# Kernel optimization log

Hardware: AMD Instinct MI355X
Metric: run time of the kernel (lower is better)

Reference implementation:

```python
import jax, jax.numpy as jnp
import numpy as np

N, C, F, T, H = 8, 64, 256, 256, 64


def _ln(x, g, b, eps=1e-5):
    m = x.mean(-1, keepdims=True)
    v = x.var(-1, keepdims=True)  # biased var, matches torch LayerNorm
    return (x - m) * jax.lax.rsqrt(v + eps) * g + b


def setup_inputs() -> dict:
    key = jax.random.key(0)
    ks = jax.random.split(key, 8)
    s = 1.0 / np.sqrt(C)
    return {
        "inputs": jax.random.normal(ks[0], (N, C, F, T), jnp.float32),
        "Wq": jax.random.normal(ks[1], (H, C), jnp.float32) * s,
        "bq": jnp.zeros((H,), jnp.float32),
        "Wk": jax.random.normal(ks[2], (H, C), jnp.float32) * s,
        "bk": jnp.zeros((H,), jnp.float32),
        "Wv": jax.random.normal(ks[3], (H, C), jnp.float32) * s,
        "bv": jnp.zeros((H,), jnp.float32),
        "g1": jnp.ones((C,), jnp.float32),
        "b1": jnp.zeros((C,), jnp.float32),
        "g2": jnp.ones((H,), jnp.float32),
        "b2": jnp.zeros((H,), jnp.float32),
        "Wt": jax.random.normal(ks[4], (C, H), jnp.float32) * s,
        "bt": jnp.zeros((C,), jnp.float32),
        "g3": jnp.ones((C,), jnp.float32),
        "b3": jnp.zeros((C,), jnp.float32),
        "alpha": jnp.full((1,), 0.25, jnp.float32),
    }


def reference(inputs, Wq, bq, Wk, bk, Wv, bv, g1, b1, g2, b2, Wt, bt, g3, b3, alpha):
    n, c, f, t = inputs.shape
    # [N,C,F,T] -> [N*T, F, C]: attention over freq bins, channels as features
    x = inputs.transpose(0, 3, 2, 1).reshape(n * t, f, c)
    h = _ln(x, g1, b1)
    q = h @ Wq.T + bq  # [B, F, H]
    k = h @ Wk.T + bk
    v = h @ Wv.T + bv
    scale = 1.0 / jnp.sqrt(jnp.asarray(q.shape[-1], q.dtype))
    e = jnp.einsum('bth,bsh->bts', q, k) * scale  # [B, F, F]
    a = jax.nn.softmax(e, axis=-1)
    wv = jnp.einsum('bts,bsh->bth', a, v)
    wv = _ln(wv, g2, b2)
    out = wv @ Wt.T + bt  # [B, F, C]
    out = out.reshape(n, t, f, c)
    out = _ln(out, g3, b3)  # LayerNorm over channel dim
    out = jnp.where(out >= 0, out, alpha * out)  # PReLU (single param)
    out = out.transpose(0, 3, 2, 1)  # back to [N, C, F, T]
    return out + inputs  # dropout is identity in eval mode
```

## Files before the change

### kernel.cpp

```cpp
#include <hip/hip_runtime.h>

typedef _Float16 f16;
typedef _Float16 f16x2 __attribute__((ext_vector_type(2)));
typedef _Float16 f16x8 __attribute__((ext_vector_type(8)));
typedef float f32x16 __attribute__((ext_vector_type(16)));
typedef unsigned int u32;
typedef unsigned short u16;

#define MFMA(a, b, c) __builtin_amdgcn_mfma_f32_32x32x16_f16((a), (b), (c), 0, 0, 0)

__device__ __forceinline__ u32 pk2(float a, float b) {
  union { f16x2 h; u32 u; } x;
  x.h[0] = (f16)a; x.h[1] = (f16)b;
  return x.u;
}
__device__ __forceinline__ float2 up2(u32 u) {
  union { u32 u_; f16x2 h; } x; x.u_ = u;
  return make_float2((float)x.h[0], (float)x.h[1]);
}
__device__ __forceinline__ f16x8 mk8(u32 a, u32 b, u32 c, u32 d) {
  union { u32 u[4]; f16x8 v; } x;
  x.u[0] = a; x.u[1] = b; x.u[2] = c; x.u[3] = d;
  return x.v;
}
__device__ __forceinline__ u16 f16b(float v) {
  union { f16 h; u16 u; } x; x.h = (f16)v; return x.u;
}
__device__ __forceinline__ float ex2(float x) {
#if __has_builtin(__builtin_amdgcn_exp2f)
  return __builtin_amdgcn_exp2f(x);
#else
  return exp2f(x);
#endif
}

__device__ __forceinline__ void sp2(float a, float b, float S, u32* hi, u32* lo) {
  union { f16x2 h; u32 u; } xh, xl;
  xh.h[0] = (f16)a; xh.h[1] = (f16)b;
  float ra = (a - (float)xh.h[0]) * S;
  float rb = (b - (float)xh.h[1]) * S;
  xl.h[0] = (f16)ra; xl.h[1] = (f16)rb;
  *hi = xh.u; *lo = xl.u;
}

template<int CTRL>
__device__ __forceinline__ float dpp_add(float v) {
  int t = __builtin_amdgcn_update_dpp(0, __builtin_bit_cast(int, v), CTRL, 0xF, 0xF, true);
  return v + __builtin_bit_cast(float, t);
}
__device__ __forceinline__ float red32(float v) {
  v = dpp_add<0xB1>(v);
  v = dpp_add<0x4E>(v);
  v = dpp_add<0x141>(v);
  v = dpp_add<0x140>(v);
  int sw = __builtin_amdgcn_ds_swizzle(__builtin_bit_cast(int, v), 0x401F);
  return v + __builtin_bit_cast(float, sw);
}

__device__ __forceinline__ f16x8 xfrag(const f32x16 a, int kt1, int g5) {
  u32 u0, u1, u2, u3;
  if (kt1 == 0) {
    u0 = pk2(a[0], a[1]);   u1 = pk2(a[2], a[3]);
    u2 = pk2(a[4], a[5]);   u3 = pk2(a[6], a[7]);
  } else {
    u0 = pk2(a[8], a[9]);   u1 = pk2(a[10], a[11]);
    u2 = pk2(a[12], a[13]); u3 = pk2(a[14], a[15]);
  }
  u32 s0 = (u32)__shfl_xor((int)u0, 32);
  u32 s1 = (u32)__shfl_xor((int)u1, 32);
  u32 s2 = (u32)__shfl_xor((int)u2, 32);
  u32 s3 = (u32)__shfl_xor((int)u3, 32);
  u32 r0 = g5 ? s2 : u0;
  u32 r1 = g5 ? s3 : u1;
  u32 r2 = g5 ? u2 : s0;
  u32 r3 = g5 ? u3 : s1;
  return mk8(r0, r1, r2, r3);
}

__device__ __forceinline__ void xfrag2(const f32x16 a, int kt1, int g5,
                                       f16x8* hi, f16x8* lo, float S) {
  u32 uh[4], ul[4];
#pragma unroll
  for (int j = 0; j < 4; ++j) {
    float v0 = kt1 ? a[8 + 2 * j] : a[2 * j];
    float v1 = kt1 ? a[9 + 2 * j] : a[2 * j + 1];
    sp2(v0, v1, S, &uh[j], &ul[j]);
  }
  u32 sh[4], sl[4];
#pragma unroll
  for (int j = 0; j < 4; ++j) {
    sh[j] = (u32)__shfl_xor((int)uh[j], 32);
    sl[j] = (u32)__shfl_xor((int)ul[j], 32);
  }
  *hi = mk8(g5 ? sh[2] : uh[0], g5 ? sh[3] : uh[1],
            g5 ? uh[2] : sh[0], g5 ? uh[3] : sh[1]);
  *lo = mk8(g5 ? sl[2] : ul[0], g5 ? sl[3] : ul[1],
            g5 ? ul[2] : sl[0], g5 ? ul[3] : sl[1]);
}

__device__ __forceinline__ f16x8 ldfrag(const char* plane, int row, int kt, int g5) {
  int s = row & 15;
  int c8 = 4 * kt + 2 * g5;
  uint2 a = *(const uint2*)(plane + row * 128 + ((c8) ^ s) * 8);
  uint2 b = *(const uint2*)(plane + row * 128 + ((c8 + 1) ^ s) * 8);
  return mk8(a.x, a.y, b.x, b.y);
}

__global__ __launch_bounds__(256) void k_pre32(const float* __restrict__ inp,
                                               float* __restrict__ xws) {
  __shared__ float tile[64 * 65];
  const int bid = blockIdx.x;
  const int n = bid >> 10;
  const int rem = bid & 1023;
  const int f = rem >> 2;
  const int t0 = (rem & 3) << 6;
  const int tid = threadIdx.x;

  const int tt = tid & 63, cb = tid >> 6;
  const float* src = inp + ((size_t)n * 64 * 256 + f) * 256 + t0;
#pragma unroll
  for (int k = 0; k < 16; ++k) {
    int c = cb * 16 + k;
    tile[c * 65 + tt] = src[(size_t)c * 65536 + tt];
  }
  __syncthreads();
  const int c2 = (tid & 31) * 2, tb = tid >> 5;
#pragma unroll
  for (int k = 0; k < 8; ++k) {
    int t = tb + 8 * k;
    float2 v = make_float2(tile[c2 * 65 + t], tile[(c2 + 1) * 65 + t]);
    *(float2*)(xws + ((size_t)(n * 256 + t0 + t) * 256 + f) * 64 + c2) = v;
  }
}

__global__ __launch_bounds__(512, 2) void k_attn(
    const float* __restrict__ xg,
    u16* __restrict__ yws,
    const float* __restrict__ Wq, const float* __restrict__ bq,
    const float* __restrict__ Wk, const float* __restrict__ bk,
    const float* __restrict__ Wv, const float* __restrict__ bv,
    const float* __restrict__ g1, const float* __restrict__ b1,
    const float* __restrict__ g2, const float* __restrict__ b2,
    const float* __restrict__ Wt, const float* __restrict__ bt,
    const float* __restrict__ g3, const float* __restrict__ b3,
    const float* __restrict__ alp) {
  extern __shared__ char smem[];
  char* Khi = smem;
  char* Klo = smem + 32768;
  char* Vlds = smem + 65536;
  char* WkH = smem + 98304;
  char* WkL = smem + 106496;
  char* WvH = smem + 114688;
  char* WvL = smem + 122880;
  char* WqH = smem + 131072;
  char* WqL = smem + 139264;
  char* WtH = smem + 147456;

  const int tid = threadIdx.x;
  const int w = tid >> 6;
  const int lane = tid & 63;
  const int l31 = lane & 31;
  const int g5 = lane >> 5;
  const int l7 = l31 & 7;
  const int b = blockIdx.x;
  const float* xb = xg + (size_t)b * 16384;
  const float RLO = 1.f / 512.f;

  float xv[32];
  {
    int f = 32 * w + l31;
#pragma unroll
    for (int kt = 0; kt < 4; ++kt) {
      float4 a = *(const float4*)(xb + f * 64 + 16 * kt + 8 * g5);
      float4 c = *(const float4*)(xb + f * 64 + 16 * kt + 8 * g5 + 4);
      xv[kt * 8 + 0] = a.x; xv[kt * 8 + 1] = a.y;
      xv[kt * 8 + 2] = a.z; xv[kt * 8 + 3] = a.w;
      xv[kt * 8 + 4] = c.x; xv[kt * 8 + 5] = c.y;
      xv[kt * 8 + 6] = c.z; xv[kt * 8 + 7] = c.w;
    }
  }

  {
    const int prow = tid >> 3, pc = tid & 7;
    const int ps = prow & 15;
    const int pha = (2 * pc) ^ ps, phb = (2 * pc + 1) ^ ps;
    const size_t off = (size_t)prow * 64 + pc * 8;
    {
      float4 a = *(const float4*)(Wk + off);
      float4 c = *(const float4*)(Wk + off + 4);
      u32 h0, l0, h1, l1, h2, l2, h3, l3;
      sp2(a.x, a.y, 512.f, &h0, &l0); sp2(a.z, a.w, 512.f, &h1, &l1);
      sp2(c.x, c.y, 512.f, &h2, &l2); sp2(c.z, c.w, 512.f, &h3, &l3);
      *(uint2*)(WkH + prow * 128 + pha * 8) = make_uint2(h0, h1);
      *(uint2*)(WkH + prow * 128 + phb * 8) = make_uint2(h2, h3);
      *(uint2*)(WkL + prow * 128 + pha * 8) = make_uint2(l0, l1);
      *(uint2*)(WkL + prow * 128 + phb * 8) = make_uint2(l2, l3);
    }
    {
      float4 a = *(const float4*)(Wv + off);
      float4 c = *(const float4*)(Wv + off + 4);
      u32 h0, l0, h1, l1, h2, l2, h3, l3;
      sp2(a.x, a.y, 512.f, &h0, &l0); sp2(a.z, a.w, 512.f, &h1, &l1);
      sp2(c.x, c.y, 512.f, &h2, &l2); sp2(c.z, c.w, 512.f, &h3, &l3);
      *(uint2*)(WvH + prow * 128 + pha * 8) = make_uint2(h0, h1);
      *(uint2*)(WvH + prow * 128 + phb * 8) = make_uint2(h2, h3);
      *(uint2*)(WvL + prow * 128 + pha * 8) = make_uint2(l0, l1);
      *(uint2*)(WvL + prow * 128 + phb * 8) = make_uint2(l2, l3);
    }
    {
      float4 a = *(const float4*)(Wq + off);
      float4 c = *(const float4*)(Wq + off + 4);
      u32 h0, l0, h1, l1, h2, l2, h3, l3;
      sp2(a.x, a.y, 512.f, &h0, &l0); sp2(a.z, a.w, 512.f, &h1, &l1);
      sp2(c.x, c.y, 512.f, &h2, &l2); sp2(c.z, c.w, 512.f, &h3, &l3);
      *(uint2*)(WqH + prow * 128 + pha * 8) = make_uint2(h0, h1);
      *(uint2*)(WqH + prow * 128 + phb * 8) = make_uint2(h2, h3);
      *(uint2*)(WqL + prow * 128 + pha * 8) = make_uint2(l0, l1);
      *(uint2*)(WqL + prow * 128 + phb * 8) = make_uint2(l2, l3);
    }
    {
      float4 a = *(const float4*)(Wt + off);
      float4 c = *(const float4*)(Wt + off + 4);
      *(uint2*)(WtH + prow * 128 + pha * 8) = make_uint2(pk2(a.x, a.y), pk2(a.z, a.w));
      *(uint2*)(WtH + prow * 128 + phb * 8) = make_uint2(pk2(c.x, c.y), pk2(c.z, c.w));
    }
  }
  __syncthreads();

  f16x8 hhi[4], hlo[4];
  {
    float s = 0.f, sq = 0.f;
#pragma unroll
    for (int i = 0; i < 32; ++i) { s += xv[i]; sq += xv[i] * xv[i]; }
    s += __shfl_xor(s, 32);
    sq += __shfl_xor(sq, 32);
    float mean = s * (1.f / 64.f);
    float var = sq * (1.f / 64.f) - mean * mean;
    float rs = rsqrtf(var + 1e-5f);
#pragma unroll
    for (int kt = 0; kt < 4; ++kt) {
      int c0 = 16 * kt + 8 * g5;
      u32 ph[4], pl[4];
#pragma unroll
      for (int j = 0; j < 4; ++j) {
        float v0 = (xv[kt * 8 + 2 * j] - mean) * rs * g1[c0 + 2 * j] + b1[c0 + 2 * j];
        float v1 = (xv[kt * 8 + 2 * j + 1] - mean) * rs * g1[c0 + 2 * j + 1] + b1[c0 + 2 * j + 1];
        sp2(v0, v1, 512.f, &ph[j], &pl[j]);
      }
      hhi[kt] = mk8(ph[0], ph[1], ph[2], ph[3]);
      hlo[kt] = mk8(pl[0], pl[1], pl[2], pl[3]);
    }
  }

  {
    f32x16 ah[2] = {}, al[2] = {};
#pragma unroll
    for (int kt = 0; kt < 4; ++kt) {
#pragma unroll
      for (int ot = 0; ot < 2; ++ot) {
        f16x8 mh = ldfrag(WkH, l31 + 32 * ot, kt, g5);
        f16x8 ml = ldfrag(WkL, l31 + 32 * ot, kt, g5);
        __builtin_amdgcn_s_setprio(1);
        ah[ot] = MFMA(mh, hhi[kt], ah[ot]);
        al[ot] = MFMA(mh, hlo[kt], al[ot]);
        al[ot] = MFMA(ml, hhi[kt], al[ot]);
        __builtin_amdgcn_s_setprio(0);
      }
    }
    int fk = 32 * w + l31;
    int sw = l7;
#pragma unroll
    for (int ot = 0; ot < 2; ++ot) {
#pragma unroll
      for (int rq = 0; rq < 4; ++rq) {
        int o0 = 32 * ot + 8 * rq + 4 * g5;
        float4 bb = *(const float4*)(bk + o0);
        float k0 = ah[ot][4 * rq + 0] + al[ot][4 * rq + 0] * RLO + bb.x;
        float k1 = ah[ot][4 * rq + 1] + al[ot][4 * rq + 1] * RLO + bb.y;
        float k2 = ah[ot][4 * rq + 2] + al[ot][4 * rq + 2] * RLO + bb.z;
        float k3 = ah[ot][4 * rq + 3] + al[ot][4 * rq + 3] * RLO + bb.w;
        u32 h01, l01, h23, l23;
        sp2(k0, k1, 512.f, &h01, &l01);
        sp2(k2, k3, 512.f, &h23, &l23);
        int ch = (4 * ot + rq) ^ sw;
        *(uint2*)(Khi + fk * 128 + ch * 16 + 8 * g5) = make_uint2(h01, h23);
        *(uint2*)(Klo + fk * 128 + ch * 16 + 8 * g5) = make_uint2(l01, l23);
      }
    }
  }

  {
    f32x16 ah[2] = {}, al[2] = {};
#pragma unroll
    for (int kt = 0; kt < 4; ++kt) {
#pragma unroll
      for (int nt = 0; nt < 2; ++nt) {
        f16x8 mh = ldfrag(WvH, l31 + 32 * nt, kt, g5);
        f16x8 ml = ldfrag(WvL, l31 + 32 * nt, kt, g5);
        __builtin_amdgcn_s_setprio(1);
        ah[nt] = MFMA(hhi[kt], mh, ah[nt]);
        al[nt] = MFMA(hlo[kt], mh, al[nt]);
        al[nt] = MFMA(hhi[kt], ml, al[nt]);
        __builtin_amdgcn_s_setprio(0);
      }
    }
#pragma unroll
    for (int nt = 0; nt < 2; ++nt) {
      int hh = l31 + 32 * nt;
      float bvj = bv[hh];
      int sw = hh & 7;
#pragma unroll
      for (int rq = 0; rq < 4; ++rq) {
        float v0 = ah[nt][4 * rq + 0] + al[nt][4 * rq + 0] * RLO + bvj;
        float v1 = ah[nt][4 * rq + 1] + al[nt][4 * rq + 1] * RLO + bvj;
        float v2 = ah[nt][4 * rq + 2] + al[nt][4 * rq + 2] * RLO + bvj;
        float v3 = ah[nt][4 * rq + 3] + al[nt][4 * rq + 3] * RLO + bvj;
        int ch = (4 * w + rq) ^ sw;
        *(uint2*)(Vlds + hh * 512 + ch * 16 + 8 * g5) =
            make_uint2(pk2(v0, v1), pk2(v2, v3));
      }
    }
  }

  f16x8 qf[4], ql[4];
  {
    f32x16 ah[2] = {}, al[2] = {};
#pragma unroll
    for (int kt = 0; kt < 4; ++kt) {
#pragma unroll
      for (int ot = 0; ot < 2; ++ot) {
        f16x8 mh = ldfrag(WqH, l31 + 32 * ot, kt, g5);
        f16x8 ml = ldfrag(WqL, l31 + 32 * ot, kt, g5);
        __builtin_amdgcn_s_setprio(1);
        ah[ot] = MFMA(mh, hhi[kt], ah[ot]);
        al[ot] = MFMA(mh, hlo[kt], al[ot]);
        al[ot] = MFMA(ml, hhi[kt], al[ot]);
        __builtin_amdgcn_s_setprio(0);
      }
    }
    const float qs = 0.18033688011112042f;
#pragma unroll
    for (int ot = 0; ot < 2; ++ot) {
#pragma unroll
      for (int rq = 0; rq < 4; ++rq) {
        int o0 = 32 * ot + 8 * rq + 4 * g5;
        float4 bb = *(const float4*)(bq + o0);
        ah[ot][4 * rq + 0] = (ah[ot][4 * rq + 0] + al[ot][4 * rq + 0] * RLO + bb.x) * qs;
        ah[ot][4 * rq + 1] = (ah[ot][4 * rq + 1] + al[ot][4 * rq + 1] * RLO + bb.y) * qs;
        ah[ot][4 * rq + 2] = (ah[ot][4 * rq + 2] + al[ot][4 * rq + 2] * RLO + bb.z) * qs;
        ah[ot][4 * rq + 3] = (ah[ot][4 * rq + 3] + al[ot][4 * rq + 3] * RLO + bb.w) * qs;
      }
    }
#pragma unroll
    for (int kt = 0; kt < 4; ++kt)
      xfrag2(ah[kt >> 1], kt & 1, g5, &qf[kt], &ql[kt], 512.f);
  }

  __syncthreads();

  const float alv = alp[0];
  const float btc0 = bt[l31], btc1 = bt[l31 + 32];
  const float g3v0 = g3[l31], g3v1 = g3[l31 + 32];
  const float b3v0 = b3[l31], b3v1 = b3[l31 + 32];
  u16* yb = yws + (size_t)b * 16384;

  f32x16 e[8];
#pragma unroll
  for (int m = 0; m < 8; ++m) {
    const char* krh = Khi + (l31 + 32 * m) * 128;
    const char* krl = Klo + (l31 + 32 * m) * 128;
    f32x16 eh = {}, em = {};
#pragma unroll
    for (int kt = 0; kt < 4; ++kt) {
      int ch = (2 * kt + g5) ^ l7;
      f16x8 kh = __builtin_bit_cast(f16x8, *(const uint4*)(krh + ch * 16));
      f16x8 kl = __builtin_bit_cast(f16x8, *(const uint4*)(krl + ch * 16));
      __builtin_amdgcn_s_setprio(1);
      eh = MFMA(kh, qf[kt], eh);
      em = MFMA(kh, ql[kt], em);
      em = MFMA(kl, qf[kt], em);
      __builtin_amdgcn_s_setprio(0);
    }
#pragma unroll
    for (int r = 0; r < 16; ++r) e[m][r] = eh[r] + em[r] * RLO;
  }
  float mx = -3.0e38f;
#pragma unroll
  for (int m = 0; m < 8; ++m)
#pragma unroll
    for (int r = 0; r < 16; ++r) mx = fmaxf(mx, e[m][r]);
  mx = fmaxf(mx, __shfl_xor(mx, 32));
  float s = 0.f;
#pragma unroll
  for (int m = 0; m < 8; ++m)
#pragma unroll
    for (int r = 0; r < 16; ++r) {
      float p = ex2(e[m][r] - mx);
      e[m][r] = p;
      s += p;
    }
  s += __shfl_xor(s, 32);
  float rcps = 1.0f / s;

  f32x16 wv0 = {}, wv1 = {};
#pragma unroll
  for (int kt = 0; kt < 16; ++kt) {
    f16x8 pf = xfrag(e[kt >> 1], kt & 1, g5);
    int ch = (2 * kt + g5) ^ l7;
    f16x8 vaf = __builtin_bit_cast(f16x8, *(const uint4*)(Vlds + l31 * 512 + ch * 16));
    f16x8 vbf = __builtin_bit_cast(f16x8, *(const uint4*)(Vlds + (l31 + 32) * 512 + ch * 16));
    __builtin_amdgcn_s_setprio(1);
    wv0 = MFMA(vaf, pf, wv0);
    wv1 = MFMA(vbf, pf, wv1);
    __builtin_amdgcn_s_setprio(0);
  }

  float s2 = 0.f, sq2 = 0.f;
#pragma unroll
  for (int r = 0; r < 16; ++r) {
    float a = wv0[r] * rcps; wv0[r] = a; s2 += a; sq2 += a * a;
    float c = wv1[r] * rcps; wv1[r] = c; s2 += c; sq2 += c * c;
  }
  s2 += __shfl_xor(s2, 32);
  sq2 += __shfl_xor(sq2, 32);
  float m2 = s2 * (1.f / 64.f);
  float v2 = sq2 * (1.f / 64.f) - m2 * m2;
  float rs2 = rsqrtf(v2 + 1e-5f);
#pragma unroll
  for (int at = 0; at < 2; ++at) {
#pragma unroll
    for (int rq = 0; rq < 4; ++rq) {
      int h0 = 32 * at + 8 * rq + 4 * g5;
      float4 gg = *(const float4*)(g2 + h0);
      float4 bb = *(const float4*)(b2 + h0);
      f32x16& a = at ? wv1 : wv0;
      a[4 * rq + 0] = (a[4 * rq + 0] - m2) * rs2 * gg.x + bb.x;
      a[4 * rq + 1] = (a[4 * rq + 1] - m2) * rs2 * gg.y + bb.y;
      a[4 * rq + 2] = (a[4 * rq + 2] - m2) * rs2 * gg.z + bb.z;
      a[4 * rq + 3] = (a[4 * rq + 3] - m2) * rs2 * gg.w + bb.w;
    }
  }
  f16x8 afh[4], afl[4];
  xfrag2(wv0, 0, g5, &afh[0], &afl[0], 1.f);
  xfrag2(wv0, 1, g5, &afh[1], &afl[1], 1.f);
  xfrag2(wv1, 0, g5, &afh[2], &afl[2], 1.f);
  xfrag2(wv1, 1, g5, &afh[3], &afl[3], 1.f);

  f32x16 o0 = {}, o1 = {};
#pragma unroll
  for (int kt = 0; kt < 4; ++kt) {
    f16x8 w0 = ldfrag(WtH, l31, kt, g5);
    f16x8 w1 = ldfrag(WtH, l31 + 32, kt, g5);
    __builtin_amdgcn_s_setprio(1);
    o0 = MFMA(afh[kt], w0, o0);
    o0 = MFMA(afl[kt], w0, o0);
    o1 = MFMA(afh[kt], w1, o1);
    o1 = MFMA(afl[kt], w1, o1);
    __builtin_amdgcn_s_setprio(0);
  }

  const int fbase = 32 * w + 4 * g5;
#pragma unroll
  for (int r = 0; r < 16; ++r) {
    float v0 = o0[r] + btc0;
    float v1 = o1[r] + btc1;
    float S = red32(v0 + v1);
    float SQ = red32(v0 * v0 + v1 * v1);
    float m3 = S * (1.f / 64.f);
    float va = SQ * (1.f / 64.f) - m3 * m3;
    float rs3 = rsqrtf(va + 1e-5f);
    float y0 = (v0 - m3) * rs3 * g3v0 + b3v0;
    float y1 = (v1 - m3) * rs3 * g3v1 + b3v1;
    y0 = y0 >= 0.f ? y0 : alv * y0;
    y1 = y1 >= 0.f ? y1 : alv * y1;
    int f = fbase + (r & 3) + 8 * (r >> 2);
    u16* yp = yb + f * 64 + l31;
    yp[0] = f16b(y0);
    yp[32] = f16b(y1);
  }
}

__global__ __launch_bounds__(256) void k_post(const float* __restrict__ inp,
                                              const u16* __restrict__ yws,
                                              float* __restrict__ out) {
  __shared__ float tile[64 * 66];
  const int bid = blockIdx.x;
  const int n = bid >> 10;
  const int rem = bid & 1023;
  const int f = rem >> 2;
  const int t0 = (rem & 3) << 6;
  const int tid = threadIdx.x;

  const int c2 = (tid & 31) * 2, tb = tid >> 5;
  const u32* src = (const u32*)yws;
#pragma unroll
  for (int k = 0; k < 8; ++k) {
    int t = tb + 8 * k;
    u32 v = src[((n * 256 + t0 + t) * 256 + f) * 32 + (tid & 31)];
    float2 p = up2(v);
    tile[t * 66 + c2] = p.x;
    tile[t * 66 + c2 + 1] = p.y;
  }
  __syncthreads();
  const int tt = tid & 63, cb = tid >> 6;
#pragma unroll
  for (int k = 0; k < 16; ++k) {
    int c = cb * 16 + k;
    size_t idx = ((size_t)(n * 64 + c) * 256 + f) * 256 + t0 + tt;
    out[idx] = inp[idx] + tile[tt * 66 + c];
  }
}

extern "C" void kernel_launch(void* const* d_in, const int* in_sizes, int n_in,
                              void* d_out, int out_size, void* d_ws, size_t ws_size,
                              hipStream_t stream) {
  const float* inp = (const float*)d_in[0];
  const float* Wq = (const float*)d_in[1];
  const float* bq = (const float*)d_in[2];
  const float* Wk = (const float*)d_in[3];
  const float* bk = (const float*)d_in[4];
  const float* Wv = (const float*)d_in[5];
  const float* bv = (const float*)d_in[6];
  const float* g1 = (const float*)d_in[7];
  const float* b1 = (const float*)d_in[8];
  const float* g2 = (const float*)d_in[9];
  const float* b2 = (const float*)d_in[10];
  const float* Wt = (const float*)d_in[11];
  const float* bt = (const float*)d_in[12];
  const float* g3 = (const float*)d_in[13];
  const float* b3 = (const float*)d_in[14];
  const float* al = (const float*)d_in[15];
  float* xstage = (float*)d_out;
  u16* yws = (u16*)d_ws;

  (void)hipFuncSetAttribute((const void*)k_attn,
                            hipFuncAttributeMaxDynamicSharedMemorySize, 155648);
  k_pre32<<<8192, 256, 0, stream>>>(inp, xstage);
  k_attn<<<2048, 512, 155648, stream>>>(xstage, yws, Wq, bq, Wk, bk, Wv, bv,
                                        g1, b1, g2, b2, Wt, bt, g3, b3, al);
  k_post<<<8192, 256, 0, stream>>>(inp, yws, (float*)d_out);
}
```

Baseline: 278.8 us.

## Make attention blocks persistent over eight batches with next-input register prefetch

The attention kernel now launches 256 blocks, and each block loops over eight consecutive sequences instead of handling one. Weight staging into shared memory (split hi/lo fp16) happens once per block rather than once per sequence. The next sequence's input rows are loaded into registers while the current one's QKV projections run. The cost is an extra barrier per iteration, higher register pressure from the prefetch, and only 256 blocks, which gives one wave of blocks with less latency hiding across blocks.

```diff
diff --git a/kernel.cpp b/kernel.cpp
--- a/kernel.cpp
+++ b/kernel.cpp
@@ -162,17 +162,16 @@
   const int l31 = lane & 31;
   const int g5 = lane >> 5;
   const int l7 = l31 & 7;
-  const int b = blockIdx.x;
-  const float* xb = xg + (size_t)b * 16384;
   const float RLO = 1.f / 512.f;
+  const int frow = 32 * w + l31;
 
   float xv[32];
   {
-    int f = 32 * w + l31;
+    const float* xb = xg + (size_t)(blockIdx.x * 8) * 16384;
 #pragma unroll
     for (int kt = 0; kt < 4; ++kt) {
-      float4 a = *(const float4*)(xb + f * 64 + 16 * kt + 8 * g5);
-      float4 c = *(const float4*)(xb + f * 64 + 16 * kt + 8 * g5 + 4);
+      float4 a = *(const float4*)(xb + frow * 64 + 16 * kt + 8 * g5);
+      float4 c = *(const float4*)(xb + frow * 64 + 16 * kt + 8 * g5 + 4);
       xv[kt * 8 + 0] = a.x; xv[kt * 8 + 1] = a.y;
       xv[kt * 8 + 2] = a.z; xv[kt * 8 + 3] = a.w;
       xv[kt * 8 + 4] = c.x; xv[kt * 8 + 5] = c.y;
@@ -227,256 +226,275 @@
   }
   __syncthreads();
 
-  f16x8 hhi[4], hlo[4];
-  {
-    float s = 0.f, sq = 0.f;
-#pragma unroll
-    for (int i = 0; i < 32; ++i) { s += xv[i]; sq += xv[i] * xv[i]; }
-    s += __shfl_xor(s, 32);
-    sq += __shfl_xor(sq, 32);
-    float mean = s * (1.f / 64.f);
-    float var = sq * (1.f / 64.f) - mean * mean;
-    float rs = rsqrtf(var + 1e-5f);
-#pragma unroll
-    for (int kt = 0; kt < 4; ++kt) {
-      int c0 = 16 * kt + 8 * g5;
-      u32 ph[4], pl[4];
-#pragma unroll
-      for (int j = 0; j < 4; ++j) {
-        float v0 = (xv[kt * 8 + 2 * j] - mean) * rs * g1[c0 + 2 * j] + b1[c0 + 2 * j];
-        float v1 = (xv[kt * 8 + 2 * j + 1] - mean) * rs * g1[c0 + 2 * j + 1] + b1[c0 + 2 * j + 1];
-        sp2(v0, v1, 512.f, &ph[j], &pl[j]);
-      }
-      hhi[kt] = mk8(ph[0], ph[1], ph[2], ph[3]);
-      hlo[kt] = mk8(pl[0], pl[1], pl[2], pl[3]);
-    }
-  }
-
-  {
-    f32x16 ah[2] = {}, al[2] = {};
-#pragma unroll
-    for (int kt = 0; kt < 4; ++kt) {
-#pragma unroll
-      for (int ot = 0; ot < 2; ++ot) {
-        f16x8 mh = ldfrag(WkH, l31 + 32 * ot, kt, g5);
-        f16x8 ml = ldfrag(WkL, l31 + 32 * ot, kt, g5);
-        __builtin_amdgcn_s_setprio(1);
-        ah[ot] = MFMA(mh, hhi[kt], ah[ot]);
-        al[ot] = MFMA(mh, hlo[kt], al[ot]);
-        al[ot] = MFMA(ml, hhi[kt], al[ot]);
-        __builtin_amdgcn_s_setprio(0);
-      }
-    }
-    int fk = 32 * w + l31;
-    int sw = l7;
-#pragma unroll
-    for (int ot = 0; ot < 2; ++ot) {
-#pragma unroll
-      for (int rq = 0; rq < 4; ++rq) {
-        int o0 = 32 * ot + 8 * rq + 4 * g5;
-        float4 bb = *(const float4*)(bk + o0);
-        float k0 = ah[ot][4 * rq + 0] + al[ot][4 * rq + 0] * RLO + bb.x;
-        float k1 = ah[ot][4 * rq + 1] + al[ot][4 * rq + 1] * RLO + bb.y;
-        float k2 = ah[ot][4 * rq + 2] + al[ot][4 * rq + 2] * RLO + bb.z;
-        float k3 = ah[ot][4 * rq + 3] + al[ot][4 * rq + 3] * RLO + bb.w;
-        u32 h01, l01, h23, l23;
-        sp2(k0, k1, 512.f, &h01, &l01);
-        sp2(k2, k3, 512.f, &h23, &l23);
-        int ch = (4 * ot + rq) ^ sw;
-        *(uint2*)(Khi + fk * 128 + ch * 16 + 8 * g5) = make_uint2(h01, h23);
-        *(uint2*)(Klo + fk * 128 + ch * 16 + 8 * g5) = make_uint2(l01, l23);
-      }
-    }
-  }
-
-  {
-    f32x16 ah[2] = {}, al[2] = {};
-#pragma unroll
-    for (int kt = 0; kt < 4; ++kt) {
-#pragma unroll
-      for (int nt = 0; nt < 2; ++nt) {
-        f16x8 mh = ldfrag(WvH, l31 + 32 * nt, kt, g5);
-        f16x8 ml = ldfrag(WvL, l31 + 32 * nt, kt, g5);
-        __builtin_amdgcn_s_setprio(1);
-        ah[nt] = MFMA(hhi[kt], mh, ah[nt]);
-        al[nt] = MFMA(hlo[kt], mh, al[nt]);
-        al[nt] = MFMA(hhi[kt], ml, al[nt]);
-        __builtin_amdgcn_s_setprio(0);
-      }
-    }
-#pragma unroll
-    for (int nt = 0; nt < 2; ++nt) {
-      int hh = l31 + 32 * nt;
-      float bvj = bv[hh];
-      int sw = hh & 7;
-#pragma unroll
-      for (int rq = 0; rq < 4; ++rq) {
-        float v0 = ah[nt][4 * rq + 0] + al[nt][4 * rq + 0] * RLO + bvj;
-        float v1 = ah[nt][4 * rq + 1] + al[nt][4 * rq + 1] * RLO + bvj;
-        float v2 = ah[nt][4 * rq + 2] + al[nt][4 * rq + 2] * RLO + bvj;
-        float v3 = ah[nt][4 * rq + 3] + al[nt][4 * rq + 3] * RLO + bvj;
-        int ch = (4 * w + rq) ^ sw;
-        *(uint2*)(Vlds + hh * 512 + ch * 16 + 8 * g5) =
-            make_uint2(pk2(v0, v1), pk2(v2, v3));
-      }
-    }
-  }
-
-  f16x8 qf[4], ql[4];
-  {
-    f32x16 ah[2] = {}, al[2] = {};
-#pragma unroll
-    for (int kt = 0; kt < 4; ++kt) {
-#pragma unroll
-      for (int ot = 0; ot < 2; ++ot) {
-        f16x8 mh = ldfrag(WqH, l31 + 32 * ot, kt, g5);
-        f16x8 ml = ldfrag(WqL, l31 + 32 * ot, kt, g5);
-        __builtin_amdgcn_s_setprio(1);
-        ah[ot] = MFMA(mh, hhi[kt], ah[ot]);
-        al[ot] = MFMA(mh, hlo[kt], al[ot]);
-        al[ot] = MFMA(ml, hhi[kt], al[ot]);
-        __builtin_amdgcn_s_setprio(0);
-      }
-    }
-    const float qs = 0.18033688011112042f;
-#pragma unroll
-    for (int ot = 0; ot < 2; ++ot) {
-#pragma unroll
-      for (int rq = 0; rq < 4; ++rq) {
-        int o0 = 32 * ot + 8 * rq + 4 * g5;
-        float4 bb = *(const float4*)(bq + o0);
-        ah[ot][4 * rq + 0] = (ah[ot][4 * rq + 0] + al[ot][4 * rq + 0] * RLO + bb.x) * qs;
-        ah[ot][4 * rq + 1] = (ah[ot][4 * rq + 1] + al[ot][4 * rq + 1] * RLO + bb.y) * qs;
-        ah[ot][4 * rq + 2] = (ah[ot][4 * rq + 2] + al[ot][4 * rq + 2] * RLO + bb.z) * qs;
-        ah[ot][4 * rq + 3] = (ah[ot][4 * rq + 3] + al[ot][4 * rq + 3] * RLO + bb.w) * qs;
-      }
-    }
-#pragma unroll
-    for (int kt = 0; kt < 4; ++kt)
-      xfrag2(ah[kt >> 1], kt & 1, g5, &qf[kt], &ql[kt], 512.f);
-  }
-
-  __syncthreads();
-
   const float alv = alp[0];
   const float btc0 = bt[l31], btc1 = bt[l31 + 32];
   const float g3v0 = g3[l31], g3v1 = g3[l31 + 32];
   const float b3v0 = b3[l31], b3v1 = b3[l31 + 32];
-  u16* yb = yws + (size_t)b * 16384;
-
-  f32x16 e[8];
-#pragma unroll
-  for (int m = 0; m < 8; ++m) {
-    const char* krh = Khi + (l31 + 32 * m) * 128;
-    const char* krl = Klo + (l31 + 32 * m) * 128;
-    f32x16 eh = {}, em = {};
+
+  for (int jj = 0; jj < 8; ++jj) {
+    const int b = blockIdx.x * 8 + jj;
+
+    f16x8 hhi[4], hlo[4];
+    {
+      float s = 0.f, sq = 0.f;
+#pragma unroll
+      for (int i = 0; i < 32; ++i) { s += xv[i]; sq += xv[i] * xv[i]; }
+      s += __shfl_xor(s, 32);
+      sq += __shfl_xor(sq, 32);
+      float mean = s * (1.f / 64.f);
+      float var = sq * (1.f / 64.f) - mean * mean;
+      float rs = rsqrtf(var + 1e-5f);
+#pragma unroll
+      for (int kt = 0; kt < 4; ++kt) {
+        int c0 = 16 * kt + 8 * g5;
+        u32 ph[4], pl[4];
+#pragma unroll
+        for (int j = 0; j < 4; ++j) {
+          float v0 = (xv[kt * 8 + 2 * j] - mean) * rs * g1[c0 + 2 * j] + b1[c0 + 2 * j];
+          float v1 = (xv[kt * 8 + 2 * j + 1] - mean) * rs * g1[c0 + 2 * j + 1] + b1[c0 + 2 * j + 1];
+          sp2(v0, v1, 512.f, &ph[j], &pl[j]);
+        }
+        hhi[kt] = mk8(ph[0], ph[1], ph[2], ph[3]);
+        hlo[kt] = mk8(pl[0], pl[1], pl[2], pl[3]);
+      }
+    }
+
+    if (jj < 7) {
+      const float* xb = xg + (size_t)(b + 1) * 16384;
+#pragma unroll
+      for (int kt = 0; kt < 4; ++kt) {
+        float4 a = *(const float4*)(xb + frow * 64 + 16 * kt + 8 * g5);
+        float4 c = *(const float4*)(xb + frow * 64 + 16 * kt + 8 * g5 + 4);
+        xv[kt * 8 + 0] = a.x; xv[kt * 8 + 1] = a.y;
+        xv[kt * 8 + 2] = a.z; xv[kt * 8 + 3] = a.w;
+        xv[kt * 8 + 4] = c.x; xv[kt * 8 + 5] = c.y;
+        xv[kt * 8 + 6] = c.z; xv[kt * 8 + 7] = c.w;
+      }
+    }
+
+    {
+      f32x16 ah[2] = {}, al[2] = {};
+#pragma unroll
+      for (int kt = 0; kt < 4; ++kt) {
+#pragma unroll
+        for (int ot = 0; ot < 2; ++ot) {
+          f16x8 mh = ldfrag(WkH, l31 + 32 * ot, kt, g5);
+          f16x8 ml = ldfrag(WkL, l31 + 32 * ot, kt, g5);
+          __builtin_amdgcn_s_setprio(1);
+          ah[ot] = MFMA(mh, hhi[kt], ah[ot]);
+          al[ot] = MFMA(mh, hlo[kt], al[ot]);
+          al[ot] = MFMA(ml, hhi[kt], al[ot]);
+          __builtin_amdgcn_s_setprio(0);
+        }
+      }
+      int sw = l7;
+#pragma unroll
+      for (int ot = 0; ot < 2; ++ot) {
+#pragma unroll
+        for (int rq = 0; rq < 4; ++rq) {
+          int o0 = 32 * ot + 8 * rq + 4 * g5;
+          float4 bb = *(const float4*)(bk + o0);
+          float k0 = ah[ot][4 * rq + 0] + al[ot][4 * rq + 0] * RLO + bb.x;
+          float k1 = ah[ot][4 * rq + 1] + al[ot][4 * rq + 1] * RLO + bb.y;
+          float k2 = ah[ot][4 * rq + 2] + al[ot][4 * rq + 2] * RLO + bb.z;
+          float k3 = ah[ot][4 * rq + 3] + al[ot][4 * rq + 3] * RLO + bb.w;
+          u32 h01, l01, h23, l23;
+          sp2(k0, k1, 512.f, &h01, &l01);
+          sp2(k2, k3, 512.f, &h23, &l23);
+          int ch = (4 * ot + rq) ^ sw;
+          *(uint2*)(Khi + frow * 128 + ch * 16 + 8 * g5) = make_uint2(h01, h23);
+          *(uint2*)(Klo + frow * 128 + ch * 16 + 8 * g5) = make_uint2(l01, l23);
+        }
+      }
+    }
+
+    {
+      f32x16 ah[2] = {}, al[2] = {};
+#pragma unroll
+      for (int kt = 0; kt < 4; ++kt) {
+#pragma unroll
+        for (int nt = 0; nt < 2; ++nt) {
+          f16x8 mh = ldfrag(WvH, l31 + 32 * nt, kt, g5);
+          f16x8 ml = ldfrag(WvL, l31 + 32 * nt, kt, g5);
+          __builtin_amdgcn_s_setprio(1);
+          ah[nt] = MFMA(hhi[kt], mh, ah[nt]);
+          al[nt] = MFMA(hlo[kt], mh, al[nt]);
+          al[nt] = MFMA(hhi[kt], ml, al[nt]);
+          __builtin_amdgcn_s_setprio(0);
+        }
+      }
+#pragma unroll
+      for (int nt = 0; nt < 2; ++nt) {
+        int hh = l31 + 32 * nt;
+        float bvj = bv[hh];
+        int sw = hh & 7;
+#pragma unroll
+        for (int rq = 0; rq < 4; ++rq) {
+          float v0 = ah[nt][4 * rq + 0] + al[nt][4 * rq + 0] * RLO + bvj;
+          float v1 = ah[nt][4 * rq + 1] + al[nt][4 * rq + 1] * RLO + bvj;
+          float v2 = ah[nt][4 * rq + 2] + al[nt][4 * rq + 2] * RLO + bvj;
+          float v3 = ah[nt][4 * rq + 3] + al[nt][4 * rq + 3] * RLO + bvj;
+          int ch = (4 * w + rq) ^ sw;
+          *(uint2*)(Vlds + hh * 512 + ch * 16 + 8 * g5) =
+              make_uint2(pk2(v0, v1), pk2(v2, v3));
+        }
+      }
+    }
+
+    f16x8 qf[4], ql[4];
+    {
+      f32x16 ah[2] = {}, al[2] = {};
+#pragma unroll
+      for (int kt = 0; kt < 4; ++kt) {
+#pragma unroll
+        for (int ot = 0; ot < 2; ++ot) {
+          f16x8 mh = ldfrag(WqH, l31 + 32 * ot, kt, g5);
+          f16x8 ml = ldfrag(WqL, l31 + 32 * ot, kt, g5);
+          __builtin_amdgcn_s_setprio(1);
+          ah[ot] = MFMA(mh, hhi[kt], ah[ot]);
+          al[ot] = MFMA(mh, hlo[kt], al[ot]);
+          al[ot] = MFMA(ml, hhi[kt], al[ot]);
+          __builtin_amdgcn_s_setprio(0);
+        }
+      }
+      const float qs = 0.18033688011112042f;
+#pragma unroll
+      for (int ot = 0; ot < 2; ++ot) {
+#pragma unroll
+        for (int rq = 0; rq < 4; ++rq) {
+          int o0 = 32 * ot + 8 * rq + 4 * g5;
+          float4 bb = *(const float4*)(bq + o0);
+          ah[ot][4 * rq + 0] = (ah[ot][4 * rq + 0] + al[ot][4 * rq + 0] * RLO + bb.x) * qs;
+          ah[ot][4 * rq + 1] = (ah[ot][4 * rq + 1] + al[ot][4 * rq + 1] * RLO + bb.y) * qs;
+          ah[ot][4 * rq + 2] = (ah[ot][4 * rq + 2] + al[ot][4 * rq + 2] * RLO + bb.z) * qs;
+          ah[ot][4 * rq + 3] = (ah[ot][4 * rq + 3] + al[ot][4 * rq + 3] * RLO + bb.w) * qs;
+        }
+      }
+#pragma unroll
+      for (int kt = 0; kt < 4; ++kt)
+        xfrag2(ah[kt >> 1], kt & 1, g5, &qf[kt], &ql[kt], 512.f);
+    }
+
+    __syncthreads();
+
+    u16* yb = yws + (size_t)b * 16384;
+
+    f32x16 e[8];
+#pragma unroll
+    for (int m = 0; m < 8; ++m) {
+      const char* krh = Khi + (l31 + 32 * m) * 128;
+      const char* krl = Klo + (l31 + 32 * m) * 128;
+      f32x16 eh = {}, em = {};
+#pragma unroll
+      for (int kt = 0; kt < 4; ++kt) {
+        int ch = (2 * kt + g5) ^ l7;
+        f16x8 kh = __builtin_bit_cast(f16x8, *(const uint4*)(krh + ch * 16));
+        f16x8 kl = __builtin_bit_cast(f16x8, *(const uint4*)(krl + ch * 16));
+        __builtin_amdgcn_s_setprio(1);
+        eh = MFMA(kh, qf[kt], eh);
+        em = MFMA(kh, ql[kt], em);
+        em = MFMA(kl, qf[kt], em);
+        __builtin_amdgcn_s_setprio(0);
+      }
+#pragma unroll
+      for (int r = 0; r < 16; ++r) e[m][r] = eh[r] + em[r] * RLO;
+    }
+    float mx = -3.0e38f;
+#pragma unroll
+    for (int m = 0; m < 8; ++m)
+#pragma unroll
+      for (int r = 0; r < 16; ++r) mx = fmaxf(mx, e[m][r]);
+    mx = fmaxf(mx, __shfl_xor(mx, 32));
+    float s = 0.f;
+#pragma unroll
+    for (int m = 0; m < 8; ++m)
+#pragma unroll
+      for (int r = 0; r < 16; ++r) {
+        float p = ex2(e[m][r] - mx);
+        e[m][r] = p;
+        s += p;
+      }
+    s += __shfl_xor(s, 32);
+    float rcps = 1.0f / s;
+
+    f32x16 wv0 = {}, wv1 = {};
+#pragma unroll
+    for (int kt = 0; kt < 16; ++kt) {
+      f16x8 pf = xfrag(e[kt >> 1], kt & 1, g5);
+      int ch = (2 * kt + g5) ^ l7;
+      f16x8 vaf = __builtin_bit_cast(f16x8, *(const uint4*)(Vlds + l31 * 512 + ch * 16));
+      f16x8 vbf = __builtin_bit_cast(f16x8, *(const uint4*)(Vlds + (l31 + 32) * 512 + ch * 16));
+      __builtin_amdgcn_s_setprio(1);
+      wv0 = MFMA(vaf, pf, wv0);
+      wv1 = MFMA(vbf, pf, wv1);
+      __builtin_amdgcn_s_setprio(0);
+    }
+
+    float s2 = 0.f, sq2 = 0.f;
+#pragma unroll
+    for (int r = 0; r < 16; ++r) {
+      float a = wv0[r] * rcps; wv0[r] = a; s2 += a; sq2 += a * a;
+      float c = wv1[r] * rcps; wv1[r] = c; s2 += c; sq2 += c * c;
+    }
+    s2 += __shfl_xor(s2, 32);
+    sq2 += __shfl_xor(sq2, 32);
+    float m2 = s2 * (1.f / 64.f);
+    float v2 = sq2 * (1.f / 64.f) - m2 * m2;
+    float rs2 = rsqrtf(v2 + 1e-5f);
+#pragma unroll
+    for (int at = 0; at < 2; ++at) {
+#pragma unroll
+      for (int rq = 0; rq < 4; ++rq) {
+        int h0 = 32 * at + 8 * rq + 4 * g5;
+        float4 gg = *(const float4*)(g2 + h0);
+        float4 bb = *(const float4*)(b2 + h0);
+        f32x16& a = at ? wv1 : wv0;
+        a[4 * rq + 0] = (a[4 * rq + 0] - m2) * rs2 * gg.x + bb.x;
+        a[4 * rq + 1] = (a[4 * rq + 1] - m2) * rs2 * gg.y + bb.y;
+        a[4 * rq + 2] = (a[4 * rq + 2] - m2) * rs2 * gg.z + bb.z;
+        a[4 * rq + 3] = (a[4 * rq + 3] - m2) * rs2 * gg.w + bb.w;
+      }
+    }
+    f16x8 afh[4], afl[4];
+    xfrag2(wv0, 0, g5, &afh[0], &afl[0], 1.f);
+    xfrag2(wv0, 1, g5, &afh[1], &afl[1], 1.f);
+    xfrag2(wv1, 0, g5, &afh[2], &afl[2], 1.f);
+    xfrag2(wv1, 1, g5, &afh[3], &afl[3], 1.f);
+
+    f32x16 o0 = {}, o1 = {};
 #pragma unroll
     for (int kt = 0; kt < 4; ++kt) {
-      int ch = (2 * kt + g5) ^ l7;
-      f16x8 kh = __builtin_bit_cast(f16x8, *(const uint4*)(krh + ch * 16));
-      f16x8 kl = __builtin_bit_cast(f16x8, *(const uint4*)(krl + ch * 16));
+      f16x8 w0 = ldfrag(WtH, l31, kt, g5);
+      f16x8 w1 = ldfrag(WtH, l31 + 32, kt, g5);
       __builtin_amdgcn_s_setprio(1);
-      eh = MFMA(kh, qf[kt], eh);
-      em = MFMA(kh, ql[kt], em);
-      em = MFMA(kl, qf[kt], em);
+      o0 = MFMA(afh[kt], w0, o0);
+      o0 = MFMA(afl[kt], w0, o0);
+      o1 = MFMA(afh[kt], w1, o1);
+      o1 = MFMA(afl[kt], w1, o1);
       __builtin_amdgcn_s_setprio(0);
     }
-#pragma unroll
-    for (int r = 0; r < 16; ++r) e[m][r] = eh[r] + em[r] * RLO;
-  }
-  float mx = -3.0e38f;
-#pragma unroll
-  for (int m = 0; m < 8; ++m)
-#pragma unroll
-    for (int r = 0; r < 16; ++r) mx = fmaxf(mx, e[m][r]);
-  mx = fmaxf(mx, __shfl_xor(mx, 32));
-  float s = 0.f;
-#pragma unroll
-  for (int m = 0; m < 8; ++m)
+
+    const int fbase = 32 * w + 4 * g5;
 #pragma unroll
     for (int r = 0; r < 16; ++r) {
-      float p = ex2(e[m][r] - mx);
-      e[m][r] = p;
-      s += p;
-    }
-  s += __shfl_xor(s, 32);
-  float rcps = 1.0f / s;
-
-  f32x16 wv0 = {}, wv1 = {};
-#pragma unroll
-  for (int kt = 0; kt < 16; ++kt) {
-    f16x8 pf = xfrag(e[kt >> 1], kt & 1, g5);
-    int ch = (2 * kt + g5) ^ l7;
-    f16x8 vaf = __builtin_bit_cast(f16x8, *(const uint4*)(Vlds + l31 * 512 + ch * 16));
-    f16x8 vbf = __builtin_bit_cast(f16x8, *(const uint4*)(Vlds + (l31 + 32) * 512 + ch * 16));
-    __builtin_amdgcn_s_setprio(1);
-    wv0 = MFMA(vaf, pf, wv0);
-    wv1 = MFMA(vbf, pf, wv1);
-    __builtin_amdgcn_s_setprio(0);
-  }
-
-  float s2 = 0.f, sq2 = 0.f;
-#pragma unroll
-  for (int r = 0; r < 16; ++r) {
-    float a = wv0[r] * rcps; wv0[r] = a; s2 += a; sq2 += a * a;
-    float c = wv1[r] * rcps; wv1[r] = c; s2 += c; sq2 += c * c;
-  }
-  s2 += __shfl_xor(s2, 32);
-  sq2 += __shfl_xor(sq2, 32);
-  float m2 = s2 * (1.f / 64.f);
-  float v2 = sq2 * (1.f / 64.f) - m2 * m2;
-  float rs2 = rsqrtf(v2 + 1e-5f);
-#pragma unroll
-  for (int at = 0; at < 2; ++at) {
-#pragma unroll
-    for (int rq = 0; rq < 4; ++rq) {
-      int h0 = 32 * at + 8 * rq + 4 * g5;
-      float4 gg = *(const float4*)(g2 + h0);
-      float4 bb = *(const float4*)(b2 + h0);
-      f32x16& a = at ? wv1 : wv0;
-      a[4 * rq + 0] = (a[4 * rq + 0] - m2) * rs2 * gg.x + bb.x;
-      a[4 * rq + 1] = (a[4 * rq + 1] - m2) * rs2 * gg.y + bb.y;
-      a[4 * rq + 2] = (a[4 * rq + 2] - m2) * rs2 * gg.z + bb.z;
-      a[4 * rq + 3] = (a[4 * rq + 3] - m2) * rs2 * gg.w + bb.w;
-    }
-  }
-  f16x8 afh[4], afl[4];
-  xfrag2(wv0, 0, g5, &afh[0], &afl[0], 1.f);
-  xfrag2(wv0, 1, g5, &afh[1], &afl[1], 1.f);
-  xfrag2(wv1, 0, g5, &afh[2], &afl[2], 1.f);
-  xfrag2(wv1, 1, g5, &afh[3], &afl[3], 1.f);
-
-  f32x16 o0 = {}, o1 = {};
-#pragma unroll
-  for (int kt = 0; kt < 4; ++kt) {
-    f16x8 w0 = ldfrag(WtH, l31, kt, g5);
-    f16x8 w1 = ldfrag(WtH, l31 + 32, kt, g5);
-    __builtin_amdgcn_s_setprio(1);
-    o0 = MFMA(afh[kt], w0, o0);
-    o0 = MFMA(afl[kt], w0, o0);
-    o1 = MFMA(afh[kt], w1, o1);
-    o1 = MFMA(afl[kt], w1, o1);
-    __builtin_amdgcn_s_setprio(0);
-  }
-
-  const int fbase = 32 * w + 4 * g5;
-#pragma unroll
-  for (int r = 0; r < 16; ++r) {
-    float v0 = o0[r] + btc0;
-    float v1 = o1[r] + btc1;
-    float S = red32(v0 + v1);
-    float SQ = red32(v0 * v0 + v1 * v1);
-    float m3 = S * (1.f / 64.f);
-    float va = SQ * (1.f / 64.f) - m3 * m3;
-    float rs3 = rsqrtf(va + 1e-5f);
-    float y0 = (v0 - m3) * rs3 * g3v0 + b3v0;
-    float y1 = (v1 - m3) * rs3 * g3v1 + b3v1;
-    y0 = y0 >= 0.f ? y0 : alv * y0;
-    y1 = y1 >= 0.f ? y1 : alv * y1;
-    int f = fbase + (r & 3) + 8 * (r >> 2);
-    u16* yp = yb + f * 64 + l31;
-    yp[0] = f16b(y0);
-    yp[32] = f16b(y1);
+      float v0 = o0[r] + btc0;
+      float v1 = o1[r] + btc1;
+      float S = red32(v0 + v1);
+      float SQ = red32(v0 * v0 + v1 * v1);
+      float m3 = S * (1.f / 64.f);
+      float va = SQ * (1.f / 64.f) - m3 * m3;
+      float rs3 = rsqrtf(va + 1e-5f);
+      float y0 = (v0 - m3) * rs3 * g3v0 + b3v0;
+      float y1 = (v1 - m3) * rs3 * g3v1 + b3v1;
+      y0 = y0 >= 0.f ? y0 : alv * y0;
+      y1 = y1 >= 0.f ? y1 : alv * y1;
+      int f = fbase + (r & 3) + 8 * (r >> 2);
+      u16* yp = yb + f * 64 + l31;
+      yp[0] = f16b(y0);
+      yp[32] = f16b(y1);
+    }
+
+    __syncthreads();
   }
 }
 
@@ -536,7 +554,7 @@
   (void)hipFuncSetAttribute((const void*)k_attn,
                             hipFuncAttributeMaxDynamicSharedMemorySize, 155648);
   k_pre32<<<8192, 256, 0, stream>>>(inp, xstage);
-  k_attn<<<2048, 512, 155648, stream>>>(xstage, yws, Wq, bq, Wk, bk, Wv, bv,
-                                        g1, b1, g2, b2, Wt, bt, g3, b3, al);
+  k_attn<<<256, 512, 155648, stream>>>(xstage, yws, Wq, bq, Wk, bk, Wv, bv,
+                                       g1, b1, g2, b2, Wt, bt, g3, b3, al);
   k_post<<<8192, 256, 0, stream>>>(inp, yws, (float*)d_out);
 }
```

Result: slower. 559.5 us (+100.7%).
